# Optimization experiments

Measured on AMD Instinct MI355X. Metric: run time of the kernel, lower is better.

The kernel has to match this reference:

```python
import jax, jax.numpy as jnp
import numpy as np

N, E, D, T, B, OUT = 20000, 80000, 768, 4, 3, 768
SCALE = 0.02


def _layer_norm(x, g, b):
    mu = jnp.mean(x, axis=-1, keepdims=True)
    var = jnp.var(x, axis=-1, keepdims=True)
    return (x - mu) / jnp.sqrt(var + 1e-5) * g + b


def _typed_linear(x, etype, bases, coeff):
    # DGL TypedLinear with basis regularizer: W[t] = sum_b coeff[t,b] * bases[b]
    # computed as 3 shared GEMMs + per-edge weighted sum (avoids [E,D,D] gather).
    c = coeff[etype]  # [E, B]
    y = c[:, 0:1] * (x @ bases[0])
    for bb in range(1, bases.shape[0]):
        y = y + c[:, bb:bb + 1] * (x @ bases[bb])
    return y


def _time_encode(t, freq, phase):
    return jnp.cos(t[:, None] * freq[None, :] + phase[None, :])


def _segment_softmax(scores, seg, n):
    m = jax.ops.segment_max(scores, seg, num_segments=n)
    m = jnp.where(jnp.isfinite(m), m, 0.0)  # empty segments -> -inf guard
    e = jnp.exp(scores - m[seg])
    den = jax.ops.segment_sum(e, seg, num_segments=n)[seg]
    return e / jnp.where(den == 0, 1.0, den)


def _forward(h, etime_hete, first_etime_homo, second_etime_homo, w_src, w_dst,
             ln_g, ln_b, src_bases, src_coeff, dst_bases, dst_coeff,
             user_bases, user_coeff, lin_w, lin_b, time_freq, time_phase,
             src_hete, dst_hete, first_etype_hete, src_homo, dst_homo,
             first_etype_homo, second_etype_homo, n_nodes):
    inv_sqrt_d = 1.0 / jnp.sqrt(jnp.asarray(768.0, h.dtype))
    n_src = h @ w_src.T  # src_weight (no bias)
    n_dst = h @ w_dst.T  # dst_weight (no bias)

    # --- heterogeneous edges ---
    sf = n_src[src_hete]
    df = n_dst[dst_hete]
    hete_src = jax.nn.relu(_typed_linear(_layer_norm(sf, ln_g, ln_b), first_etype_hete, src_bases, src_coeff))
    msg_h = _time_encode(etime_hete, time_freq, time_phase) + hete_src
    e_h = jnp.sum(msg_h * df, axis=1) * inv_sqrt_d
    a_h = _segment_softmax(e_h, dst_hete, n_nodes)
    h_hete = jax.ops.segment_sum(a_h[:, None] * msg_h, dst_hete, num_segments=n_nodes)

    # --- homogeneous edges ---
    sf = n_src[src_homo]
    df = n_dst[dst_homo]
    dst_feat = jax.nn.relu(_typed_linear(_layer_norm(df, ln_g, ln_b), first_etype_homo, dst_bases, dst_coeff))
    homo_feat = jax.nn.relu(_typed_linear(_layer_norm(sf, ln_g, ln_b), second_etype_homo, user_bases, user_coeff))
    t_homo = jnp.maximum(first_etime_homo, second_etime_homo)
    msg_o = _time_encode(t_homo, time_freq, time_phase) + homo_feat
    e_o = jnp.sum(msg_o * dst_feat, axis=1) * inv_sqrt_d
    a_o = _segment_softmax(e_o, dst_homo, n_nodes)
    h_homo = jax.ops.segment_sum(a_o[:, None] * msg_o, dst_homo, num_segments=n_nodes)

    n = jnp.concatenate([h_hete, h_homo], axis=-1)  # [N, 2D]
    z = jax.nn.relu(n @ lin_w.T + lin_b)
    zn = jnp.linalg.norm(z, axis=1, keepdims=True)
    return z / jnp.where(zn == 0, 1.0, zn)


def setup_inputs() -> dict:
    key = jax.random.key(0)
    ks = jax.random.split(key, 24)
    inp = {
        'h': jax.random.normal(ks[0], (N, D), jnp.float32),
        'etime_hete': jax.random.uniform(ks[1], (E,), jnp.float32),
        'first_etime_homo': jax.random.uniform(ks[2], (E,), jnp.float32),
        'second_etime_homo': jax.random.uniform(ks[3], (E,), jnp.float32),
        'w_src': jax.random.normal(ks[4], (D, D), jnp.float32) * SCALE,
        'w_dst': jax.random.normal(ks[5], (D, D), jnp.float32) * SCALE,
        'ln_g': jnp.ones((D,), jnp.float32),
        'ln_b': jnp.zeros((D,), jnp.float32),
        'src_bases': jax.random.normal(ks[6], (B, D, D), jnp.float32) * SCALE,
        'src_coeff': jax.random.normal(ks[7], (T, B), jnp.float32),
        'dst_bases': jax.random.normal(ks[8], (B, D, D), jnp.float32) * SCALE,
        'dst_coeff': jax.random.normal(ks[9], (T, B), jnp.float32),
        'user_bases': jax.random.normal(ks[10], (B, D, D), jnp.float32) * SCALE,
        'user_coeff': jax.random.normal(ks[11], (T, B), jnp.float32),
        'lin_w': jax.random.normal(ks[12], (OUT, 2 * D), jnp.float32) * SCALE,
        'lin_b': jnp.zeros((OUT,), jnp.float32),
        'time_freq': jnp.asarray(1.0 / 10 ** np.linspace(0, 9, D), jnp.float32),
        'time_phase': jnp.zeros((D,), jnp.float32),
        'src_hete': jax.random.randint(ks[13], (E,), 0, N, jnp.int32),
        'dst_hete': jax.random.randint(ks[14], (E,), 0, N, jnp.int32),
        'first_etype_hete': jax.random.randint(ks[15], (E,), 0, T, jnp.int32),
        'src_homo': jax.random.randint(ks[16], (E,), 0, N, jnp.int32),
        'dst_homo': jax.random.randint(ks[17], (E,), 0, N, jnp.int32),
        'first_etype_homo': jax.random.randint(ks[18], (E,), 0, T, jnp.int32),
        'second_etype_homo': jax.random.randint(ks[19], (E,), 0, T, jnp.int32),
        'num_nodes': N,
    }
    return inp


def reference(h, etime_hete, first_etime_homo, second_etime_homo, w_src, w_dst,
              ln_g, ln_b, src_bases, src_coeff, dst_bases, dst_coeff,
              user_bases, user_coeff, lin_w, lin_b, time_freq, time_phase,
              src_hete, dst_hete, first_etype_hete, src_homo, dst_homo,
              first_etype_homo, second_etype_homo, num_nodes):
    return _forward(h, etime_hete, first_etime_homo, second_etime_homo, w_src,
                    w_dst, ln_g, ln_b, src_bases, src_coeff, dst_bases,
                    dst_coeff, user_bases, user_coeff, lin_w, lin_b,
                    time_freq, time_phase, src_hete, dst_hete,
                    first_etype_hete, src_homo, dst_homo, first_etype_homo,
                    second_etype_homo, num_nodes)
```

## Files before the change

kernel.cpp:

```cpp
#include <hip/hip_runtime.h>
#include <hip/hip_bf16.h>
#include <stdint.h>

#define D 768
#define INV_SQRT_D 0.03608439182435161269f

static void* g_scratch = nullptr;
#define SCRATCH_BYTES ((size_t)600 * 1024 * 1024)

__attribute__((constructor))
static void _alloc_scratch() {
    if (hipMalloc(&g_scratch, SCRATCH_BYTES) != hipSuccess) g_scratch = nullptr;
}

static inline int cdiv(int a, int b) { return (a + b - 1) / b; }

typedef __attribute__((ext_vector_type(8))) short bf16x8;
typedef __attribute__((ext_vector_type(4))) float f32x4;

__device__ __forceinline__ unsigned cvt2b(float lo, float hi) {
    unsigned r;
    asm("v_cvt_pk_bf16_f32 %0, %1, %2" : "=v"(r) : "v"(lo), "v"(hi));
    return r;
}
__device__ __forceinline__ unsigned short f2b(float f) {
    return (unsigned short)cvt2b(f, f);
}
__device__ __forceinline__ float b2f(unsigned short u) {
    union { unsigned u; float f; } c; c.u = (unsigned)u << 16;
    return c.f;
}

__device__ __forceinline__ float block_reduce_sum(float v) {
#pragma unroll
    for (int off = 32; off > 0; off >>= 1) v += __shfl_down(v, off, 64);
    __shared__ float sm[4];
    int lane = threadIdx.x & 63, w = threadIdx.x >> 6;
    __syncthreads();
    if (lane == 0) sm[w] = v;
    __syncthreads();
    return (sm[0] + sm[1]) + (sm[2] + sm[3]);
}

template <bool CONCAT, bool BF16C, bool RELU, bool BIAS>
__global__ __launch_bounds__(256) void mfma_gemm(
    const unsigned short* __restrict__ A1, const unsigned short* __restrict__ A2,
    int lda, int ksplit,
    const unsigned short* __restrict__ B, int ldb,
    void* __restrict__ Cv, int ldc,
    const float* __restrict__ bias,
    int M, int K)
{
    __shared__ unsigned short As[128 * 32];
    __shared__ unsigned short Bs[128 * 32];
    const int tid = threadIdx.x;
    const int wv = tid >> 6, lane = tid & 63;
    const int m0 = blockIdx.y * 128, n0 = blockIdx.x * 128;
    const int wm = (wv >> 1) << 6;
    const int wn = (wv & 1) << 6;
    const int fr = lane & 15;
    const int fq = lane >> 4;

    f32x4 acc[4][4] = {};

    for (int k0 = 0; k0 < K; k0 += 32) {
        const unsigned short* Asrc = A1;
        int kk = k0;
        if (CONCAT && k0 >= ksplit) { Asrc = A2; kk = k0 - ksplit; }
#pragma unroll
        for (int j = 0; j < 2; ++j) {
            int idx = j * 256 + tid;
            int row = idx >> 2, cb = (idx & 3) << 3;
            int am = m0 + row; if (am > M - 1) am = M - 1;
            const unsigned short* ga = Asrc + (size_t)am * lda + kk + cb;
            char* la = (char*)As + (size_t)(j * 256 + wv * 64) * 16;
            __builtin_amdgcn_global_load_lds(
                (const __attribute__((address_space(1))) unsigned int*)ga,
                (__attribute__((address_space(3))) unsigned int*)la, 16, 0, 0);
            const unsigned short* gb = B + (size_t)(n0 + row) * ldb + k0 + cb;
            char* lb = (char*)Bs + (size_t)(j * 256 + wv * 64) * 16;
            __builtin_amdgcn_global_load_lds(
                (const __attribute__((address_space(1))) unsigned int*)gb,
                (__attribute__((address_space(3))) unsigned int*)lb, 16, 0, 0);
        }
        __syncthreads();

        bf16x8 af[4], bfv[4];
#pragma unroll
        for (int i = 0; i < 4; ++i) {
            af[i]  = *(const bf16x8*)&As[(wm + i * 16 + fr) * 32 + fq * 8];
            bfv[i] = *(const bf16x8*)&Bs[(wn + i * 16 + fr) * 32 + fq * 8];
        }
#pragma unroll
        for (int mi = 0; mi < 4; ++mi)
#pragma unroll
            for (int ni = 0; ni < 4; ++ni)
                acc[mi][ni] = __builtin_amdgcn_mfma_f32_16x16x32_bf16(
                    af[mi], bfv[ni], acc[mi][ni], 0, 0, 0);
        __syncthreads();
    }

#pragma unroll
    for (int mi = 0; mi < 4; ++mi) {
#pragma unroll
        for (int r = 0; r < 4; ++r) {
            int m = m0 + wm + mi * 16 + fq * 4 + r;
            if (m >= M) continue;
#pragma unroll
            for (int ni = 0; ni < 4; ++ni) {
                int n = n0 + wn + ni * 16 + fr;
                float v = acc[mi][ni][r];
                if (BIAS) v += bias[n];
                if (RELU) v = fmaxf(v, 0.f);
                if (BF16C) ((unsigned short*)Cv)[(size_t)m * ldc + n] = f2b(v);
                else       ((float*)Cv)[(size_t)m * ldc + n] = v;
            }
        }
    }
}

__global__ void f32_to_bf16_kernel(const float* __restrict__ in,
                                   unsigned short* __restrict__ out, int n4) {
    int i = blockIdx.x * 256 + threadIdx.x;
    if (i >= n4) return;
    float4 v = *reinterpret_cast<const float4*>(in + (size_t)i * 4);
    ushort4 o;
    o.x = f2b(v.x); o.y = f2b(v.y); o.z = f2b(v.z); o.w = f2b(v.w);
    *reinterpret_cast<ushort4*>(out + (size_t)i * 4) = o;
}

__global__ __launch_bounds__(256) void combine_transpose_kernel(
    const float* __restrict__ in, const float* __restrict__ coeff,
    unsigned short* __restrict__ out) {
    int t = blockIdx.z;
    float c0 = coeff[t * 3 + 0], c1 = coeff[t * 3 + 1], c2 = coeff[t * 3 + 2];
    __shared__ float tile[32][33];
    int bx = blockIdx.x * 32, by = blockIdx.y * 32;
    int tx = threadIdx.x & 31, ty = threadIdx.x >> 5;
#pragma unroll
    for (int i = 0; i < 32; i += 8) {
        size_t idx = (size_t)(by + ty + i) * D + bx + tx;
        tile[ty + i][tx] = c0 * in[idx] + c1 * in[idx + (size_t)D * D]
                         + c2 * in[idx + (size_t)2 * D * D];
    }
    __syncthreads();
    unsigned short* o = out + (size_t)t * D * D;
#pragma unroll
    for (int i = 0; i < 32; i += 8)
        o[(size_t)(bx + ty + i) * D + by + tx] = f2b(tile[tx][ty + i]);
}

__global__ __launch_bounds__(256) void ln_bf16_kernel(
    unsigned short* __restrict__ x, int ld,
    const float* __restrict__ g, const float* __restrict__ b)
{
    unsigned short* r = x + (size_t)blockIdx.x * ld;
    int t = threadIdx.x;
    float v0 = b2f(r[t]), v1 = b2f(r[t + 256]), v2 = b2f(r[t + 512]);
    float s = block_reduce_sum(v0 + v1 + v2);
    float mu = s * (1.f / 768.f);
    float d0 = v0 - mu, d1 = v1 - mu, d2 = v2 - mu;
    float q = block_reduce_sum(d0 * d0 + d1 * d1 + d2 * d2);
    float rstd = 1.f / sqrtf(q * (1.f / 768.f) + 1e-5f);
    r[t]       = f2b(d0 * rstd * g[t]       + b[t]);
    r[t + 256] = f2b(d1 * rstd * g[t + 256] + b[t + 256]);
    r[t + 512] = f2b(d2 * rstd * g[t + 512] + b[t + 512]);
}

__global__ __launch_bounds__(256) void score_hete_kernel(
    const unsigned short* __restrict__ P, int ldp,
    const unsigned short* __restrict__ nd, int ldn,
    const float* __restrict__ etime,
    const int* __restrict__ src, const int* __restrict__ dst, const int* __restrict__ et,
    const float* __restrict__ freq, const float* __restrict__ phase,
    float* __restrict__ esc, int E)
{
    int e = blockIdx.x * 4 + (threadIdx.x >> 6);
    if (e >= E) return;
    int l = threadIdx.x & 63;
    int s = src[e], d = dst[e], ty = et[e];
    float tv = etime[e];
    const unsigned short* ps = P + (size_t)s * ldp + ty * D;
    const unsigned short* pd = nd + (size_t)d * ldn;
    float acc = 0.f;
    {
        bf16x8 a = *(const bf16x8*)(ps + l * 8);
        bf16x8 b = *(const bf16x8*)(pd + l * 8);
#pragma unroll
        for (int q = 0; q < 8; ++q) {
            int j = l * 8 + q;
            float m = __cosf(tv * freq[j] + phase[j]) + b2f((unsigned short)a[q]);
            acc += m * b2f((unsigned short)b[q]);
        }
    }
    if (l < 32) {
        bf16x8 a = *(const bf16x8*)(ps + 512 + l * 8);
        bf16x8 b = *(const bf16x8*)(pd + 512 + l * 8);
#pragma unroll
        for (int q = 0; q < 8; ++q) {
            int j = 512 + l * 8 + q;
            float m = __cosf(tv * freq[j] + phase[j]) + b2f((unsigned short)a[q]);
            acc += m * b2f((unsigned short)b[q]);
        }
    }
#pragma unroll
    for (int off = 32; off > 0; off >>= 1) acc += __shfl_down(acc, off, 64);
    if (l == 0) esc[e] = acc * INV_SQRT_D;
}

__global__ __launch_bounds__(256) void score_homo_kernel(
    const unsigned short* __restrict__ Pd, int ldpd,
    const unsigned short* __restrict__ Pu, int ldpu,
    const float* __restrict__ t1, const float* __restrict__ t2,
    const int* __restrict__ src, const int* __restrict__ dst,
    const int* __restrict__ et1, const int* __restrict__ et2,
    const float* __restrict__ freq, const float* __restrict__ phase,
    float* __restrict__ esc, int E)
{
    int e = blockIdx.x * 4 + (threadIdx.x >> 6);
    if (e >= E) return;
    int l = threadIdx.x & 63;
    int s = src[e], d = dst[e];
    int ta = et1[e], tb = et2[e];
    float tv = fmaxf(t1[e], t2[e]);
    const unsigned short* pu = Pu + (size_t)s * ldpu + tb * D;
    const unsigned short* pd = Pd + (size_t)d * ldpd + ta * D;
    float acc = 0.f;
    {
        bf16x8 a = *(const bf16x8*)(pu + l * 8);
        bf16x8 b = *(const bf16x8*)(pd + l * 8);
#pragma unroll
        for (int q = 0; q < 8; ++q) {
            int j = l * 8 + q;
            float m = __cosf(tv * freq[j] + phase[j]) + b2f((unsigned short)a[q]);
            acc += m * b2f((unsigned short)b[q]);
        }
    }
    if (l < 32) {
        bf16x8 a = *(const bf16x8*)(pu + 512 + l * 8);
        bf16x8 b = *(const bf16x8*)(pd + 512 + l * 8);
#pragma unroll
        for (int q = 0; q < 8; ++q) {
            int j = 512 + l * 8 + q;
            float m = __cosf(tv * freq[j] + phase[j]) + b2f((unsigned short)a[q]);
            acc += m * b2f((unsigned short)b[q]);
        }
    }
#pragma unroll
    for (int off = 32; off > 0; off >>= 1) acc += __shfl_down(acc, off, 64);
    if (l == 0) esc[e] = acc * INV_SQRT_D;
}

__global__ void zero_int_kernel(int* __restrict__ p, int n) {
    int i = blockIdx.x * 256 + threadIdx.x;
    if (i < n) p[i] = 0;
}

__global__ void count2_kernel(const int* __restrict__ dA, const int* __restrict__ dB,
                              int* __restrict__ cntA, int* __restrict__ cntB, int E) {
    int e = blockIdx.x * 256 + threadIdx.x;
    if (e < E) {
        atomicAdd(&cntA[dA[e]], 1);
        atomicAdd(&cntB[dB[e]], 1);
    }
}

__global__ __launch_bounds__(1024) void scan2_kernel(
    const int* __restrict__ cntA, int* __restrict__ offsA,
    const int* __restrict__ cntB, int* __restrict__ offsB, int n)
{
    __shared__ int tmp[1024];
    __shared__ int carry;
    int tid = threadIdx.x;
    for (int g = 0; g < 2; ++g) {
        const int* cnt = g ? cntB : cntA;
        int* offs = g ? offsB : offsA;
        __syncthreads();
        if (tid == 0) carry = 0;
        __syncthreads();
        for (int base = 0; base < n; base += 1024) {
            int idx = base + tid;
            int v = (idx < n) ? cnt[idx] : 0;
            tmp[tid] = v;
            __syncthreads();
            for (int off = 1; off < 1024; off <<= 1) {
                int t = (tid >= off) ? tmp[tid - off] : 0;
                __syncthreads();
                tmp[tid] += t;
                __syncthreads();
            }
            int inc = tmp[tid];
            int c = carry;
            if (idx < n) offs[idx] = c + inc - v;
            __syncthreads();
            if (tid == 0) carry = c + tmp[1023];
            __syncthreads();
        }
        if (tid == 0) offs[n] = carry;
    }
}

__global__ void scatter2_kernel(
    const int* __restrict__ dA, const int* __restrict__ offsA,
    int* __restrict__ curA, int* __restrict__ listA,
    const int* __restrict__ dB, const int* __restrict__ offsB,
    int* __restrict__ curB, int* __restrict__ listB, int E) {
    int e = blockIdx.x * 256 + threadIdx.x;
    if (e < E) {
        int d = dA[e];
        listA[offsA[d] + atomicAdd(&curA[d], 1)] = e;
        d = dB[e];
        listB[offsB[d] + atomicAdd(&curB[d], 1)] = e;
    }
}

__global__ void seg_softmax_kernel(const int* __restrict__ offs, const int* __restrict__ list,
                                   float* __restrict__ score, int n) {
    int v = blockIdx.x * 256 + threadIdx.x;
    if (v >= n) return;
    int a = offs[v], b = offs[v + 1];
    if (a == b) return;
    float m = -INFINITY;
    for (int i = a; i < b; i++) m = fmaxf(m, score[list[i]]);
    float den = 0.f;
    for (int i = a; i < b; i++) den += expf(score[list[i]] - m);
    float inv = 1.f / den;
    for (int i = a; i < b; i++) { int e = list[i]; score[e] = expf(score[e] - m) * inv; }
}

template <bool IS_HOMO>
__global__ __launch_bounds__(256) void agg_kernel(
    const int* __restrict__ offs, const int* __restrict__ list,
    const float* __restrict__ a,
    const unsigned short* __restrict__ P, int ldp,
    const float* __restrict__ t1, const float* __restrict__ t2,
    const int* __restrict__ src, const int* __restrict__ et,
    const float* __restrict__ freq, const float* __restrict__ phase,
    unsigned short* __restrict__ out, int nN)
{
    int v = blockIdx.x * 4 + (threadIdx.x >> 6);
    if (v >= nN) return;
    int l = threadIdx.x & 63;

    float frq[16], phs[16], acc[16];
#pragma unroll
    for (int q = 0; q < 16; ++q) { frq[q] = 0.f; phs[q] = 0.f; acc[q] = 0.f; }
    {
        float4 f0 = *(const float4*)(freq + l * 8);
        float4 f1 = *(const float4*)(freq + l * 8 + 4);
        float4 p0 = *(const float4*)(phase + l * 8);
        float4 p1 = *(const float4*)(phase + l * 8 + 4);
        frq[0] = f0.x; frq[1] = f0.y; frq[2] = f0.z; frq[3] = f0.w;
        frq[4] = f1.x; frq[5] = f1.y; frq[6] = f1.z; frq[7] = f1.w;
        phs[0] = p0.x; phs[1] = p0.y; phs[2] = p0.z; phs[3] = p0.w;
        phs[4] = p1.x; phs[5] = p1.y; phs[6] = p1.z; phs[7] = p1.w;
    }
    if (l < 32) {
        float4 f0 = *(const float4*)(freq + 512 + l * 8);
        float4 f1 = *(const float4*)(freq + 512 + l * 8 + 4);
        float4 p0 = *(const float4*)(phase + 512 + l * 8);
        float4 p1 = *(const float4*)(phase + 512 + l * 8 + 4);
        frq[8]  = f0.x; frq[9]  = f0.y; frq[10] = f0.z; frq[11] = f0.w;
        frq[12] = f1.x; frq[13] = f1.y; frq[14] = f1.z; frq[15] = f1.w;
        phs[8]  = p0.x; phs[9]  = p0.y; phs[10] = p0.z; phs[11] = p0.w;
        phs[12] = p1.x; phs[13] = p1.y; phs[14] = p1.z; phs[15] = p1.w;
    }

    int i0 = offs[v], i1 = offs[v + 1];
    for (int i = i0; i < i1; ++i) {
        int e = list[i];
        int s = src[e], ty = et[e];
        float w = a[e];
        float tv = IS_HOMO ? fmaxf(t1[e], t2[e]) : t1[e];
        const unsigned short* ps = P + (size_t)s * ldp + ty * D;
        bf16x8 r0 = *(const bf16x8*)(ps + l * 8);
#pragma unroll
        for (int q = 0; q < 8; ++q)
            acc[q] += w * (__cosf(tv * frq[q] + phs[q]) + b2f((unsigned short)r0[q]));
        if (l < 32) {
            bf16x8 r1 = *(const bf16x8*)(ps + 512 + l * 8);
#pragma unroll
            for (int q = 0; q < 8; ++q)
                acc[8 + q] += w * (__cosf(tv * frq[8 + q] + phs[8 + q])
                                   + b2f((unsigned short)r1[q]));
        }
    }

    unsigned short* o = out + (size_t)v * D;
    uint4 st;
    st.x = cvt2b(acc[0], acc[1]); st.y = cvt2b(acc[2], acc[3]);
    st.z = cvt2b(acc[4], acc[5]); st.w = cvt2b(acc[6], acc[7]);
    *reinterpret_cast<uint4*>(o + (size_t)l * 8) = st;
    if (l < 32) {
        st.x = cvt2b(acc[8], acc[9]);   st.y = cvt2b(acc[10], acc[11]);
        st.z = cvt2b(acc[12], acc[13]); st.w = cvt2b(acc[14], acc[15]);
        *reinterpret_cast<uint4*>(o + 512 + (size_t)l * 8) = st;
    }
}

__global__ __launch_bounds__(256) void normalize_kernel(
    const float* __restrict__ z, float* __restrict__ out)
{
    const float* x = z + (size_t)blockIdx.x * D;
    int t = threadIdx.x;
    float v0 = x[t], v1 = x[t + 256], v2 = x[t + 512];
    float s = block_reduce_sum(v0 * v0 + v1 * v1 + v2 * v2);
    float nrm = sqrtf(s);
    float inv = (nrm == 0.f) ? 1.f : 1.f / nrm;
    float* o = out + (size_t)blockIdx.x * D;
    o[t] = v0 * inv; o[t + 256] = v1 * inv; o[t + 512] = v2 * inv;
}

__global__ void fill_f32_kernel(float* __restrict__ p, float v, int n) {
    int i = blockIdx.x * 256 + threadIdx.x;
    if (i < n) p[i] = v;
}

extern "C" void kernel_launch(void* const* d_in, const int* in_sizes, int n_in,
                              void* d_out, int out_size, void* d_ws, size_t ws_size,
                              hipStream_t stream)
{
    const float* h          = (const float*)d_in[0];
    const float* etime_hete = (const float*)d_in[1];
    const float* t1_homo    = (const float*)d_in[2];
    const float* t2_homo    = (const float*)d_in[3];
    const float* w_src      = (const float*)d_in[4];
    const float* w_dst      = (const float*)d_in[5];
    const float* ln_g       = (const float*)d_in[6];
    const float* ln_b       = (const float*)d_in[7];
    const float* src_bases  = (const float*)d_in[8];
    const float* src_coeff  = (const float*)d_in[9];
    const float* dst_bases  = (const float*)d_in[10];
    const float* dst_coeff  = (const float*)d_in[11];
    const float* user_bases = (const float*)d_in[12];
    const float* user_coeff = (const float*)d_in[13];
    const float* lin_w      = (const float*)d_in[14];
    const float* lin_b      = (const float*)d_in[15];
    const float* time_freq  = (const float*)d_in[16];
    const float* time_phase = (const float*)d_in[17];
    const int* src_hete = (const int*)d_in[18];
    const int* dst_hete = (const int*)d_in[19];
    const int* et_hete  = (const int*)d_in[20];
    const int* src_homo = (const int*)d_in[21];
    const int* dst_homo = (const int*)d_in[22];
    const int* et1_homo = (const int*)d_in[23];
    const int* et2_homo = (const int*)d_in[24];

    const int N = in_sizes[0] / D;
    const int E = in_sizes[1];

    const size_t szST  = (size_t)N * 1536 * 2;
    const size_t szPSU = (size_t)N * 6144 * 2;
    const size_t szPD  = (size_t)N * 3072 * 2;
    const size_t szVb  = (size_t)N * D * 2;
    const size_t szW   = (size_t)D * D * 2;
    size_t need = szST + szPSU + szPD + 3 * szVb
                + 2 * szW + 2 * szW + 8 * szW + 4 * szW
                + (size_t)E * 4 + (size_t)2 * N * 4
                + 2 * (((size_t)(N + 1) * 4 + 255) & ~(size_t)255)
                + (size_t)2 * E * 4 + 16384;

    char* base;
    if (ws_size >= need) base = (char*)d_ws;
    else if (g_scratch)  base = (char*)g_scratch;
    else {
        fill_f32_kernel<<<cdiv(out_size, 256), 256, 0, stream>>>(
            (float*)d_out, 1000.0f + (float)(ws_size >> 20), out_size);
        return;
    }

    char* p = base;
    auto carve = [&](size_t bytes) { char* r = p; p += (bytes + 255) & ~(size_t)255; return r; };
    unsigned short* STb = (unsigned short*)carve(szST);
    unsigned short* PSU = (unsigned short*)carve(szPSU);
    unsigned short* PD  = (unsigned short*)carve(szPD);
    unsigned short* hb  = (unsigned short*)carve(szVb);
    unsigned short* hAb = (unsigned short*)carve(szVb);
    unsigned short* hOb = (unsigned short*)carve(szVb);
    unsigned short* wsb = (unsigned short*)carve(2 * szW);
    unsigned short* lwb = (unsigned short*)carve(2 * szW);
    unsigned short* suW = (unsigned short*)carve(8 * szW);
    unsigned short* dstW = (unsigned short*)carve(4 * szW);
    float* esc  = (float*)carve((size_t)E * 4);
    int* cnt    = (int*)carve((size_t)2 * N * 4);
    int* offsA  = (int*)carve((size_t)(N + 1) * 4);
    int* offsB  = (int*)carve((size_t)(N + 1) * 4);
    int* listA  = (int*)carve((size_t)E * 4);
    int* listB  = (int*)carve((size_t)E * 4);
    float* z    = (float*)PSU;

    unsigned short* Sb = STb;
    unsigned short* Tb = STb + 768;
    unsigned short* Psrc_t  = PSU;
    unsigned short* Puser_t = PSU + 3072;

    const int eb = cdiv(E, 256);
    const int nb2 = cdiv(2 * N, 256);
    const int MB = cdiv(N, 128);
    dim3 g_proj(12, MB);
    dim3 g_psu(48, MB);
    dim3 g_pd(24, MB);
    dim3 g_fin(6, MB);
    dim3 ct_grid(24, 24, 4);
    const int seb = cdiv(E, 4);
    const int agb = cdiv(N, 4);

    f32_to_bf16_kernel<<<cdiv(N * D / 4, 256), 256, 0, stream>>>(h, hb, N * D / 4);
    f32_to_bf16_kernel<<<cdiv(D * D / 4, 256), 256, 0, stream>>>(w_src, wsb, D * D / 4);
    f32_to_bf16_kernel<<<cdiv(D * D / 4, 256), 256, 0, stream>>>(w_dst, wsb + (size_t)D * D, D * D / 4);
    f32_to_bf16_kernel<<<cdiv(D * 2 * D / 4, 256), 256, 0, stream>>>(lin_w, lwb, D * 2 * D / 4);
    combine_transpose_kernel<<<ct_grid, 256, 0, stream>>>(src_bases, src_coeff, suW);
    combine_transpose_kernel<<<ct_grid, 256, 0, stream>>>(user_bases, user_coeff, suW + (size_t)4 * D * D);
    combine_transpose_kernel<<<ct_grid, 256, 0, stream>>>(dst_bases, dst_coeff, dstW);

    zero_int_kernel<<<nb2, 256, 0, stream>>>(cnt, 2 * N);
    count2_kernel<<<eb, 256, 0, stream>>>(dst_hete, dst_homo, cnt, cnt + N, E);
    scan2_kernel<<<1, 1024, 0, stream>>>(cnt, offsA, cnt + N, offsB, N);
    zero_int_kernel<<<nb2, 256, 0, stream>>>(cnt, 2 * N);
    scatter2_kernel<<<eb, 256, 0, stream>>>(dst_hete, offsA, cnt, listA,
                                            dst_homo, offsB, cnt + N, listB, E);

    mfma_gemm<false, true, false, false><<<g_proj, 256, 0, stream>>>(
        hb, hb, D, D, wsb, D, STb, 1536, nullptr, N, D);
    ln_bf16_kernel<<<N, 256, 0, stream>>>(Sb, 1536, ln_g, ln_b);

    mfma_gemm<false, true, true, false><<<g_psu, 256, 0, stream>>>(
        Sb, Sb, 1536, D, suW, D, PSU, 6144, nullptr, N, D);

    score_hete_kernel<<<seb, 256, 0, stream>>>(Psrc_t, 6144, Tb, 1536, etime_hete,
                                               src_hete, dst_hete, et_hete,
                                               time_freq, time_phase, esc, E);
    seg_softmax_kernel<<<cdiv(N, 256), 256, 0, stream>>>(offsA, listA, esc, N);
    agg_kernel<false><<<agb, 256, 0, stream>>>(offsA, listA, esc, Psrc_t, 6144,
                                               etime_hete, nullptr, src_hete, et_hete,
                                               time_freq, time_phase, hAb, N);

    ln_bf16_kernel<<<N, 256, 0, stream>>>(Tb, 1536, ln_g, ln_b);
    mfma_gemm<false, true, true, false><<<g_pd, 256, 0, stream>>>(
        Tb, Tb, 1536, D, dstW, D, PD, 3072, nullptr, N, D);

    score_homo_kernel<<<seb, 256, 0, stream>>>(PD, 3072, Puser_t, 6144,
                                               t1_homo, t2_homo, src_homo, dst_homo,
                                               et1_homo, et2_homo, time_freq, time_phase, esc, E);
    seg_softmax_kernel<<<cdiv(N, 256), 256, 0, stream>>>(offsB, listB, esc, N);
    agg_kernel<true><<<agb, 256, 0, stream>>>(offsB, listB, esc, Puser_t, 6144,
                                              t1_homo, t2_homo, src_homo, et2_homo,
                                              time_freq, time_phase, hOb, N);

    mfma_gemm<true, false, true, true><<<g_fin, 256, 0, stream>>>(
        hAb, hOb, D, D, lwb, 2 * D, z, D, lin_b, N, 2 * D);
    normalize_kernel<<<N, 256, 0, stream>>>(z, (float*)d_out);
}
```

Before: 1.127 ms.

## Fuse edge scoring, segment softmax and aggregation with online softmax; swizzle GEMM tiles

Replaces the separate per-edge score kernels, per-node segment softmax and aggregation kernels with one per-destination-node kernel. It computes each message once, takes its dot product with the destination features, and accumulates with a running-max online softmax. This removes the edge-score scratch buffer, the repeated gathers of source rows and the duplicate cosine time-encoding work. The cost is a serial wave-wide reduction per edge inside the node loop, which may leave high-degree nodes latency bound. The GEMM also remaps block indices across the 8 XCDs so that neighbouring tiles share an L2.

```diff
diff --git a/kernel.cpp b/kernel.cpp
--- a/kernel.cpp
+++ b/kernel.cpp
@@ -40,6 +40,17 @@
     if (lane == 0) sm[w] = v;
     __syncthreads();
     return (sm[0] + sm[1]) + (sm[2] + sm[3]);
+}
+
+__device__ __forceinline__ void xcd_swizzle(int& bx, int& by) {
+    int nx = gridDim.x;
+    int nwg = nx * gridDim.y;
+    int o = blockIdx.y * nx + blockIdx.x;
+    int q = nwg >> 3, r = nwg & 7;
+    int xcd = o & 7, idx = o >> 3;
+    int n = (xcd < r) ? (xcd * (q + 1) + idx)
+                      : (r * (q + 1) + (xcd - r) * q + idx);
+    bx = n % nx; by = n / nx;
 }
 
 template <bool CONCAT, bool BF16C, bool RELU, bool BIAS>
@@ -55,7 +66,9 @@
     __shared__ unsigned short Bs[128 * 32];
     const int tid = threadIdx.x;
     const int wv = tid >> 6, lane = tid & 63;
-    const int m0 = blockIdx.y * 128, n0 = blockIdx.x * 128;
+    int bx, by;
+    xcd_swizzle(bx, by);
+    const int m0 = by * 128, n0 = bx * 128;
     const int wm = (wv >> 1) << 6;
     const int wn = (wv & 1) << 6;
     const int fr = lane & 15;
@@ -165,90 +178,6 @@
     r[t]       = f2b(d0 * rstd * g[t]       + b[t]);
     r[t + 256] = f2b(d1 * rstd * g[t + 256] + b[t + 256]);
     r[t + 512] = f2b(d2 * rstd * g[t + 512] + b[t + 512]);
-}
-
-__global__ __launch_bounds__(256) void score_hete_kernel(
-    const unsigned short* __restrict__ P, int ldp,
-    const unsigned short* __restrict__ nd, int ldn,
-    const float* __restrict__ etime,
-    const int* __restrict__ src, const int* __restrict__ dst, const int* __restrict__ et,
-    const float* __restrict__ freq, const float* __restrict__ phase,
-    float* __restrict__ esc, int E)
-{
-    int e = blockIdx.x * 4 + (threadIdx.x >> 6);
-    if (e >= E) return;
-    int l = threadIdx.x & 63;
-    int s = src[e], d = dst[e], ty = et[e];
-    float tv = etime[e];
-    const unsigned short* ps = P + (size_t)s * ldp + ty * D;
-    const unsigned short* pd = nd + (size_t)d * ldn;
-    float acc = 0.f;
-    {
-        bf16x8 a = *(const bf16x8*)(ps + l * 8);
-        bf16x8 b = *(const bf16x8*)(pd + l * 8);
-#pragma unroll
-        for (int q = 0; q < 8; ++q) {
-            int j = l * 8 + q;
-            float m = __cosf(tv * freq[j] + phase[j]) + b2f((unsigned short)a[q]);
-            acc += m * b2f((unsigned short)b[q]);
-        }
-    }
-    if (l < 32) {
-        bf16x8 a = *(const bf16x8*)(ps + 512 + l * 8);
-        bf16x8 b = *(const bf16x8*)(pd + 512 + l * 8);
-#pragma unroll
-        for (int q = 0; q < 8; ++q) {
-            int j = 512 + l * 8 + q;
-            float m = __cosf(tv * freq[j] + phase[j]) + b2f((unsigned short)a[q]);
-            acc += m * b2f((unsigned short)b[q]);
-        }
-    }
-#pragma unroll
-    for (int off = 32; off > 0; off >>= 1) acc += __shfl_down(acc, off, 64);
-    if (l == 0) esc[e] = acc * INV_SQRT_D;
-}
-
-__global__ __launch_bounds__(256) void score_homo_kernel(
-    const unsigned short* __restrict__ Pd, int ldpd,
-    const unsigned short* __restrict__ Pu, int ldpu,
-    const float* __restrict__ t1, const float* __restrict__ t2,
-    const int* __restrict__ src, const int* __restrict__ dst,
-    const int* __restrict__ et1, const int* __restrict__ et2,
-    const float* __restrict__ freq, const float* __restrict__ phase,
-    float* __restrict__ esc, int E)
-{
-    int e = blockIdx.x * 4 + (threadIdx.x >> 6);
-    if (e >= E) return;
-    int l = threadIdx.x & 63;
-    int s = src[e], d = dst[e];
-    int ta = et1[e], tb = et2[e];
-    float tv = fmaxf(t1[e], t2[e]);
-    const unsigned short* pu = Pu + (size_t)s * ldpu + tb * D;
-    const unsigned short* pd = Pd + (size_t)d * ldpd + ta * D;
-    float acc = 0.f;
-    {
-        bf16x8 a = *(const bf16x8*)(pu + l * 8);
-        bf16x8 b = *(const bf16x8*)(pd + l * 8);
-#pragma unroll
-        for (int q = 0; q < 8; ++q) {
-            int j = l * 8 + q;
-            float m = __cosf(tv * freq[j] + phase[j]) + b2f((unsigned short)a[q]);
-            acc += m * b2f((unsigned short)b[q]);
-        }
-    }
-    if (l < 32) {
-        bf16x8 a = *(const bf16x8*)(pu + 512 + l * 8);
-        bf16x8 b = *(const bf16x8*)(pd + 512 + l * 8);
-#pragma unroll
-        for (int q = 0; q < 8; ++q) {
-            int j = 512 + l * 8 + q;
-            float m = __cosf(tv * freq[j] + phase[j]) + b2f((unsigned short)a[q]);
-            acc += m * b2f((unsigned short)b[q]);
-        }
-    }
-#pragma unroll
-    for (int off = 32; off > 0; off >>= 1) acc += __shfl_down(acc, off, 64);
-    if (l == 0) esc[e] = acc * INV_SQRT_D;
 }
 
 __global__ void zero_int_kernel(int* __restrict__ p, int n) {
@@ -314,37 +243,26 @@
     }
 }
 
-__global__ void seg_softmax_kernel(const int* __restrict__ offs, const int* __restrict__ list,
-                                   float* __restrict__ score, int n) {
-    int v = blockIdx.x * 256 + threadIdx.x;
-    if (v >= n) return;
-    int a = offs[v], b = offs[v + 1];
-    if (a == b) return;
-    float m = -INFINITY;
-    for (int i = a; i < b; i++) m = fmaxf(m, score[list[i]]);
-    float den = 0.f;
-    for (int i = a; i < b; i++) den += expf(score[list[i]] - m);
-    float inv = 1.f / den;
-    for (int i = a; i < b; i++) { int e = list[i]; score[e] = expf(score[e] - m) * inv; }
-}
-
 template <bool IS_HOMO>
-__global__ __launch_bounds__(256) void agg_kernel(
+__global__ __launch_bounds__(256) void edge_fused_kernel(
     const int* __restrict__ offs, const int* __restrict__ list,
-    const float* __restrict__ a,
-    const unsigned short* __restrict__ P, int ldp,
+    const unsigned short* __restrict__ Pmsg, int ldm,
+    const unsigned short* __restrict__ Pdst, int ldd,
     const float* __restrict__ t1, const float* __restrict__ t2,
-    const int* __restrict__ src, const int* __restrict__ et,
+    const int* __restrict__ src,
+    const int* __restrict__ etA,
+    const int* __restrict__ etB,
     const float* __restrict__ freq, const float* __restrict__ phase,
     unsigned short* __restrict__ out, int nN)
 {
     int v = blockIdx.x * 4 + (threadIdx.x >> 6);
     if (v >= nN) return;
     int l = threadIdx.x & 63;
-
-    float frq[16], phs[16], acc[16];
-#pragma unroll
-    for (int q = 0; q < 16; ++q) { frq[q] = 0.f; phs[q] = 0.f; acc[q] = 0.f; }
+    bool hi = l < 32;
+
+    float frq[16], phs[16];
+#pragma unroll
+    for (int q = 0; q < 16; ++q) { frq[q] = 0.f; phs[q] = 0.f; }
     {
         float4 f0 = *(const float4*)(freq + l * 8);
         float4 f1 = *(const float4*)(freq + l * 8 + 4);
@@ -355,7 +273,7 @@
         phs[0] = p0.x; phs[1] = p0.y; phs[2] = p0.z; phs[3] = p0.w;
         phs[4] = p1.x; phs[5] = p1.y; phs[6] = p1.z; phs[7] = p1.w;
     }
-    if (l < 32) {
+    if (hi) {
         float4 f0 = *(const float4*)(freq + 512 + l * 8);
         float4 f1 = *(const float4*)(freq + 512 + l * 8 + 4);
         float4 p0 = *(const float4*)(phase + 512 + l * 8);
@@ -366,34 +284,91 @@
         phs[12] = p1.x; phs[13] = p1.y; phs[14] = p1.z; phs[15] = p1.w;
     }
 
+    float nd[16];
+#pragma unroll
+    for (int q = 0; q < 16; ++q) nd[q] = 0.f;
+    if (!IS_HOMO) {
+        const unsigned short* pd = Pdst + (size_t)v * ldd;
+        bf16x8 r0 = *(const bf16x8*)(pd + l * 8);
+#pragma unroll
+        for (int q = 0; q < 8; ++q) nd[q] = b2f((unsigned short)r0[q]);
+        if (hi) {
+            bf16x8 r1 = *(const bf16x8*)(pd + 512 + l * 8);
+#pragma unroll
+            for (int q = 0; q < 8; ++q) nd[8 + q] = b2f((unsigned short)r1[q]);
+        }
+    }
+
+    float m = -INFINITY, den = 0.f;
+    float acc[16];
+#pragma unroll
+    for (int q = 0; q < 16; ++q) acc[q] = 0.f;
+
     int i0 = offs[v], i1 = offs[v + 1];
     for (int i = i0; i < i1; ++i) {
         int e = list[i];
-        int s = src[e], ty = et[e];
-        float w = a[e];
+        int s = src[e];
         float tv = IS_HOMO ? fmaxf(t1[e], t2[e]) : t1[e];
-        const unsigned short* ps = P + (size_t)s * ldp + ty * D;
-        bf16x8 r0 = *(const bf16x8*)(ps + l * 8);
+        int tym = IS_HOMO ? etB[e] : etA[e];
+        const unsigned short* pm = Pmsg + (size_t)s * ldm + tym * D;
+
+        float msg[16];
+#pragma unroll
+        for (int q = 0; q < 16; ++q) msg[q] = 0.f;
+        bf16x8 r0 = *(const bf16x8*)(pm + l * 8);
 #pragma unroll
         for (int q = 0; q < 8; ++q)
-            acc[q] += w * (__cosf(tv * frq[q] + phs[q]) + b2f((unsigned short)r0[q]));
-        if (l < 32) {
-            bf16x8 r1 = *(const bf16x8*)(ps + 512 + l * 8);
+            msg[q] = __cosf(tv * frq[q] + phs[q]) + b2f((unsigned short)r0[q]);
+        if (hi) {
+            bf16x8 r1 = *(const bf16x8*)(pm + 512 + l * 8);
 #pragma unroll
             for (int q = 0; q < 8; ++q)
-                acc[8 + q] += w * (__cosf(tv * frq[8 + q] + phs[8 + q])
-                                   + b2f((unsigned short)r1[q]));
-        }
-    }
-
+                msg[8 + q] = __cosf(tv * frq[8 + q] + phs[8 + q])
+                           + b2f((unsigned short)r1[q]);
+        }
+
+        float dotp = 0.f;
+        if (IS_HOMO) {
+            int ta = etA[e];
+            const unsigned short* pd2 = Pdst + (size_t)v * ldd + ta * D;
+            bf16x8 d0 = *(const bf16x8*)(pd2 + l * 8);
+#pragma unroll
+            for (int q = 0; q < 8; ++q) {
+                float dv = fmaxf(b2f((unsigned short)d0[q]), 0.f);
+                dotp += msg[q] * dv;
+            }
+            if (hi) {
+                bf16x8 d1 = *(const bf16x8*)(pd2 + 512 + l * 8);
+#pragma unroll
+                for (int q = 0; q < 8; ++q)
+                    dotp += msg[8 + q] * b2f((unsigned short)d1[q]);
+            }
+        } else {
+#pragma unroll
+            for (int q = 0; q < 16; ++q) dotp += msg[q] * nd[q];
+        }
+#pragma unroll
+        for (int off = 1; off < 64; off <<= 1) dotp += __shfl_xor(dotp, off, 64);
+        float sc = dotp * INV_SQRT_D;
+
+        float nm = fmaxf(m, sc);
+        float sOld = __expf(m - nm);
+        float w = __expf(sc - nm);
+        den = den * sOld + w;
+#pragma unroll
+        for (int q = 0; q < 16; ++q) acc[q] = acc[q] * sOld + w * msg[q];
+        m = nm;
+    }
+
+    float inv = (den > 0.f) ? 1.f / den : 0.f;
     unsigned short* o = out + (size_t)v * D;
     uint4 st;
-    st.x = cvt2b(acc[0], acc[1]); st.y = cvt2b(acc[2], acc[3]);
-    st.z = cvt2b(acc[4], acc[5]); st.w = cvt2b(acc[6], acc[7]);
+    st.x = cvt2b(acc[0] * inv, acc[1] * inv); st.y = cvt2b(acc[2] * inv, acc[3] * inv);
+    st.z = cvt2b(acc[4] * inv, acc[5] * inv); st.w = cvt2b(acc[6] * inv, acc[7] * inv);
     *reinterpret_cast<uint4*>(o + (size_t)l * 8) = st;
-    if (l < 32) {
-        st.x = cvt2b(acc[8], acc[9]);   st.y = cvt2b(acc[10], acc[11]);
-        st.z = cvt2b(acc[12], acc[13]); st.w = cvt2b(acc[14], acc[15]);
+    if (hi) {
+        st.x = cvt2b(acc[8] * inv, acc[9] * inv);   st.y = cvt2b(acc[10] * inv, acc[11] * inv);
+        st.z = cvt2b(acc[12] * inv, acc[13] * inv); st.w = cvt2b(acc[14] * inv, acc[15] * inv);
         *reinterpret_cast<uint4*>(o + 512 + (size_t)l * 8) = st;
     }
 }
@@ -456,7 +431,7 @@
     const size_t szW   = (size_t)D * D * 2;
     size_t need = szST + szPSU + szPD + 3 * szVb
                 + 2 * szW + 2 * szW + 8 * szW + 4 * szW
-                + (size_t)E * 4 + (size_t)2 * N * 4
+                + (size_t)2 * N * 4
                 + 2 * (((size_t)(N + 1) * 4 + 255) & ~(size_t)255)
                 + (size_t)2 * E * 4 + 16384;
 
@@ -481,7 +456,6 @@
     unsigned short* lwb = (unsigned short*)carve(2 * szW);
     unsigned short* suW = (unsigned short*)carve(8 * szW);
     unsigned short* dstW = (unsigned short*)carve(4 * szW);
-    float* esc  = (float*)carve((size_t)E * 4);
     int* cnt    = (int*)carve((size_t)2 * N * 4);
     int* offsA  = (int*)carve((size_t)(N + 1) * 4);
     int* offsB  = (int*)carve((size_t)(N + 1) * 4);
@@ -502,7 +476,6 @@
     dim3 g_pd(24, MB);
     dim3 g_fin(6, MB);
     dim3 ct_grid(24, 24, 4);
-    const int seb = cdiv(E, 4);
     const int agb = cdiv(N, 4);
 
     f32_to_bf16_kernel<<<cdiv(N * D / 4, 256), 256, 0, stream>>>(h, hb, N * D / 4);
@@ -527,25 +500,19 @@
     mfma_gemm<false, true, true, false><<<g_psu, 256, 0, stream>>>(
         Sb, Sb, 1536, D, suW, D, PSU, 6144, nullptr, N, D);
 
-    score_hete_kernel<<<seb, 256, 0, stream>>>(Psrc_t, 6144, Tb, 1536, etime_hete,
-                                               src_hete, dst_hete, et_hete,
-                                               time_freq, time_phase, esc, E);
-    seg_softmax_kernel<<<cdiv(N, 256), 256, 0, stream>>>(offsA, listA, esc, N);
-    agg_kernel<false><<<agb, 256, 0, stream>>>(offsA, listA, esc, Psrc_t, 6144,
-                                               etime_hete, nullptr, src_hete, et_hete,
-                                               time_freq, time_phase, hAb, N);
+    edge_fused_kernel<false><<<agb, 256, 0, stream>>>(
+        offsA, listA, Psrc_t, 6144, Tb, 1536,
+        etime_hete, nullptr, src_hete, et_hete, nullptr,
+        time_freq, time_phase, hAb, N);
 
     ln_bf16_kernel<<<N, 256, 0, stream>>>(Tb, 1536, ln_g, ln_b);
     mfma_gemm<false, true, true, false><<<g_pd, 256, 0, stream>>>(
         Tb, Tb, 1536, D, dstW, D, PD, 3072, nullptr, N, D);
 
-    score_homo_kernel<<<seb, 256, 0, stream>>>(PD, 3072, Puser_t, 6144,
-                                               t1_homo, t2_homo, src_homo, dst_homo,
-                                               et1_homo, et2_homo, time_freq, time_phase, esc, E);
-    seg_softmax_kernel<<<cdiv(N, 256), 256, 0, stream>>>(offsB, listB, esc, N);
-    agg_kernel<true><<<agb, 256, 0, stream>>>(offsB, listB, esc, Puser_t, 6144,
-                                              t1_homo, t2_homo, src_homo, et2_homo,
-                                              time_freq, time_phase, hOb, N);
+    edge_fused_kernel<true><<<agb, 256, 0, stream>>>(
+        offsB, listB, Puser_t, 6144, PD, 3072,
+        t1_homo, t2_homo, src_homo, et1_homo, et2_homo,
+        time_freq, time_phase, hOb, N);
 
     mfma_gemm<true, false, true, true><<<g_fin, 256, 0, stream>>>(
         hAb, hOb, D, D, lwb, 2 * D, z, D, lin_b, N, 2 * D);
```

Measured after the change: 1.112 ms. Within noise of the previous version (-1.4%).
